# Kernel tuning notes

Hardware: AMD Instinct MI355X
Metric: run time of the kernel (lower is better)

Reference implementation:

```python
import jax, jax.numpy as jnp
import numpy as np
from jax import lax

B, T, D = 4, 2048, 2048
H, K, V = 16, 128, 128
CONV_K = 4
EPS_G = 1e-6
LN_EPS = 1e-5


def _dconv_causal(x, w, b):
    # x: (B,T,C); w: (C,1,Kk) depthwise. torch pads both sides Kk-1 then slices [:T],
    # which equals a causal left-pad of Kk-1.
    y = lax.conv_general_dilated(
        jnp.transpose(x, (0, 2, 1)), w, (1,),
        [(w.shape[-1] - 1, 0)],
        dimension_numbers=('NCH', 'OIH', 'NCH'),
        feature_group_count=w.shape[0])
    return jnp.transpose(y + b[None, :, None], (0, 2, 1))


def _kda_scan(q, k, v, g, beta, scale):
    # q,k: (B,H,T,K); v: (B,H,T,V); g: (B,H,T,K) log-decay (channel-wise); beta: (B,H,T)
    # Gated delta rule: S_t = Diag(exp(g_t)) S_{t-1} + beta_t k_t (v_t - k_t^T Diag(exp(g_t)) S_{t-1})
    S0 = jnp.zeros(q.shape[:2] + (q.shape[-1], v.shape[-1]), q.dtype)

    def step(S, inp):
        qt, kt, vt, gt, bt = inp
        S = S * jnp.exp(gt)[..., :, None]                     # per-key-channel decay
        err = vt - jnp.einsum('bhk,bhkv->bhv', kt, S)         # delta correction
        S = S + bt[..., None, None] * kt[..., None] * err[..., None, :]
        o = scale * jnp.einsum('bhk,bhkv->bhv', qt, S)
        return S, o

    xs = tuple(jnp.moveaxis(t_, 2, 0) for t_ in (q, k, v, g)) + (jnp.moveaxis(beta, 2, 0),)
    _, o = lax.scan(step, S0, xs)
    return jnp.moveaxis(o, 0, 2)                              # (B,H,T,V)


def setup_inputs() -> dict:
    key = jax.random.key(0)
    ks = jax.random.split(key, 16)
    s = 0.02
    return {
        'x':   jax.random.normal(ks[0], (B, T, D), jnp.float32),
        'Wq':  jax.random.normal(ks[1], (H * K, D), jnp.float32) * s,
        'Wk':  jax.random.normal(ks[2], (H * K, D), jnp.float32) * s,
        'Wv':  jax.random.normal(ks[3], (H * V, D), jnp.float32) * s,
        'Wa':  jax.random.normal(ks[4], (H * V, D), jnp.float32) * s,
        'ba':  jax.random.normal(ks[5], (H * V,), jnp.float32) * s,
        'Wb':  jax.random.normal(ks[6], (H, D), jnp.float32) * s,
        'bb':  jax.random.normal(ks[7], (H,), jnp.float32) * s,
        'Wg':  jax.random.normal(ks[8], (H * V, D), jnp.float32) * s,
        'Wo':  jax.random.normal(ks[9], (D, H * V), jnp.float32) * s,
        'cqw': jax.random.normal(ks[10], (H * K, 1, CONV_K), jnp.float32) * 0.2,
        'cqb': jnp.zeros((H * K,), jnp.float32),
        'ckw': jax.random.normal(ks[11], (H * K, 1, CONV_K), jnp.float32) * 0.2,
        'ckb': jnp.zeros((H * K,), jnp.float32),
        'cvw': jax.random.normal(ks[12], (H * V, 1, CONV_K), jnp.float32) * 0.2,
        'cvb': jnp.zeros((H * V,), jnp.float32),
        'ln_w': jnp.ones((V,), jnp.float32),
        'ln_b': jnp.zeros((V,), jnp.float32),
    }


def reference(x, Wq, Wk, Wv, Wa, ba, Wb, bb, Wg, Wo,
              cqw, cqb, ckw, ckb, cvw, cvb, ln_w, ln_b):
    b, t, _ = x.shape
    scale = K ** -0.5
    q = jax.nn.silu(_dconv_causal(x @ Wq.T, cqw, cqb))
    k = jax.nn.silu(_dconv_causal(x @ Wk.T, ckw, ckb))
    v = jax.nn.silu(_dconv_causal(x @ Wv.T, cvw, cvb))
    q = q.reshape(b, t, H, K).transpose(0, 2, 1, 3)           # (B,H,T,K)
    k = k.reshape(b, t, H, K).transpose(0, 2, 1, 3)
    v = v.reshape(b, t, H, V).transpose(0, 2, 1, 3)
    a = jax.nn.sigmoid(x @ Wa.T + ba).reshape(b, t, H, V).transpose(0, 2, 1, 3)
    g = jnp.log(jnp.maximum(a, EPS_G))                        # log-space channel gate
    beta = jax.nn.sigmoid(x @ Wb.T + bb).transpose(0, 2, 1)   # (B,H,T)
    o = _kda_scan(q, k, v, g, beta, scale).transpose(0, 2, 1, 3)  # (B,T,H,V)
    mu = o.mean(-1, keepdims=True)
    var = ((o - mu) ** 2).mean(-1, keepdims=True)
    o = (o - mu) * lax.rsqrt(var + LN_EPS) * ln_w + ln_b      # per-head LayerNorm
    gate = jax.nn.sigmoid(x @ Wg.T).reshape(b, t, H, V)
    return ((o * gate).reshape(b, t, H * V)) @ Wo.T
```

## Files before the change

kernel.cpp:

```cpp
#include <hip/hip_runtime.h>
#include <cstdint>
#include <cstddef>

#define B_ 4
#define T_ 2048
#define D_ 2048
#define H_ 16

typedef __bf16 bf16x8 __attribute__((ext_vector_type(8)));
typedef float  f32x4  __attribute__((ext_vector_type(4)));
typedef unsigned short u16;
typedef u16 u16x8 __attribute__((ext_vector_type(8)));

__device__ __forceinline__ u16 f2bf(float f) {
    union { float f; unsigned u; } v; v.f = f;
    unsigned r = v.u + 0x7FFFu + ((v.u >> 16) & 1u);
    return (u16)(r >> 16);
}
__device__ __forceinline__ float bf2f(u16 h) {
    union { unsigned u; float f; } v; v.u = ((unsigned)h) << 16;
    return v.f;
}
__device__ __forceinline__ float sigmoidf_(float x) {
    return 1.f / (1.f + __expf(-x));
}
__device__ __forceinline__ void async_load16(const void* g, void* l) {
    __builtin_amdgcn_global_load_lds(
        (const __attribute__((address_space(1))) void*)g,
        (__attribute__((address_space(3))) void*)l,
        16, 0, 0);
}

__device__ __forceinline__ float row_allreduce16(float x) {
    int v;
    v = __builtin_amdgcn_update_dpp(0, __builtin_bit_cast(int, x), 0xB1, 0xF, 0xF, true);
    x += __builtin_bit_cast(float, v);
    v = __builtin_amdgcn_update_dpp(0, __builtin_bit_cast(int, x), 0x4E, 0xF, 0xF, true);
    x += __builtin_bit_cast(float, v);
    v = __builtin_amdgcn_update_dpp(0, __builtin_bit_cast(int, x), 0x140, 0xF, 0xF, true);
    x += __builtin_bit_cast(float, v);
    v = __builtin_amdgcn_update_dpp(0, __builtin_bit_cast(int, x), 0x141, 0xF, 0xF, true);
    x += __builtin_bit_cast(float, v);
    return x;
}

__global__ void cvt_bf16_k(const float* __restrict__ s, u16* __restrict__ d, int n) {
    int i = blockIdx.x * 256 + threadIdx.x;
    if (i * 4 < n) {
        float4 v = *(const float4*)(s + (size_t)i * 4);
        ushort4 o = {f2bf(v.x), f2bf(v.y), f2bf(v.z), f2bf(v.w)};
        *(ushort4*)(d + (size_t)i * 4) = o;
    }
}

__global__ void pad_wb_k(const float* __restrict__ Wb, u16* __restrict__ d) {
    int i = blockIdx.x * 256 + threadIdx.x;
    d[i] = (i < 32768) ? f2bf(Wb[i]) : (u16)0;
}

__device__ __forceinline__ void store_c(float* p, float v) { *p = v; }
__device__ __forceinline__ void store_c(u16* p, float v) { *p = f2bf(v); }

template <typename OutT, int PERM>
__global__ __launch_bounds__(256) void gemm_bt(const u16* __restrict__ A,
                                               const u16* __restrict__ Bm,
                                               OutT* __restrict__ C, int K, int ldc) {
    __shared__ __align__(16) u16 smA[128 * 64];
    __shared__ __align__(16) u16 smB[128 * 64];
    const int tid  = threadIdx.x;
    const int lane = tid & 63;
    const int w    = tid >> 6;
    const int wm   = (w >> 1) * 64;
    const int wn   = (w & 1) * 64;
    const int bm   = blockIdx.x, bn = blockIdx.y;

    f32x4 acc[4][4];
#pragma unroll
    for (int i = 0; i < 4; ++i)
#pragma unroll
        for (int j = 0; j < 4; ++j) acc[i][j] = (f32x4){0.f, 0.f, 0.f, 0.f};

    const int rr = tid >> 3;
    const int cc = (tid & 7) * 8;
    const u16* Ag = A + (size_t)(bm * 128) * K;
    const u16* Bg = Bm + (size_t)(bn * 128) * K;

    for (int k0 = 0; k0 < K; k0 += 64) {
#pragma unroll
        for (int it = 0; it < 4; ++it) {
            async_load16(Ag + (size_t)(it * 32 + rr) * K + (k0 + cc), &smA[(it * 256 + tid) * 8]);
            async_load16(Bg + (size_t)(it * 32 + rr) * K + (k0 + cc), &smB[(it * 256 + tid) * 8]);
        }
        __syncthreads();
#pragma unroll
        for (int kk = 0; kk < 64; kk += 32) {
            bf16x8 af[4], bfr[4];
            const int qoff = kk + ((lane >> 4) * 8);
#pragma unroll
            for (int mi = 0; mi < 4; ++mi)
                af[mi] = *(const bf16x8*)&smA[(wm + mi * 16 + (lane & 15)) * 64 + qoff];
#pragma unroll
            for (int ni = 0; ni < 4; ++ni)
                bfr[ni] = *(const bf16x8*)&smB[(wn + ni * 16 + (lane & 15)) * 64 + qoff];
#pragma unroll
            for (int mi = 0; mi < 4; ++mi)
#pragma unroll
                for (int ni = 0; ni < 4; ++ni)
                    acc[mi][ni] = __builtin_amdgcn_mfma_f32_16x16x32_bf16(af[mi], bfr[ni], acc[mi][ni], 0, 0, 0);
        }
        __syncthreads();
    }

#pragma unroll
    for (int mi = 0; mi < 4; ++mi) {
        const int row0 = bm * 128 + wm + mi * 16 + ((lane >> 4) * 4);
#pragma unroll
        for (int ni = 0; ni < 4; ++ni) {
            int colg = bn * 128 + wn + ni * 16 + (lane & 15);
            if (PERM) colg = (colg & ~127) | (((colg & 15) << 3) | ((colg >> 4) & 7));
#pragma unroll
            for (int rg = 0; rg < 4; ++rg)
                store_c(&C[(size_t)(row0 + rg) * ldc + colg], acc[mi][ni][rg]);
        }
    }
}

template <int TRANSPOSE>
__global__ void conv_silu_k(const u16* __restrict__ pre,
                            const float* __restrict__ w, const float* __restrict__ bias,
                            u16* __restrict__ outp) {
    int idx = blockIdx.x * 256 + threadIdx.x;
    int c = idx & 2047;
    int t = (idx >> 11) & (T_ - 1);
    int b = idx >> 22;
    const u16* base = pre + (size_t)(b * T_ + t) * 2048 + c;
    float acc = bias[c];
#pragma unroll
    for (int j = 0; j < 4; ++j) {
        int tt = t - 3 + j;
        if (tt >= 0) {
            float xv = bf2f(base[(ptrdiff_t)(j - 3) * 2048]);
            acc = fmaf(xv, w[c * 4 + j], acc);
        }
    }
    float y = acc * sigmoidf_(acc);
    int h = c >> 7, cl = c & 127;
    int p = TRANSPOSE ? ((cl & 15) * 8 + (cl >> 4)) : cl;
    outp[((size_t)(b * H_ + h) * T_ + t) * 128 + p] = f2bf(y);
}

#define TB2 16
__global__ __launch_bounds__(512, 2) void kda_scan_k(const u16* __restrict__ qg,
                                                     const u16* __restrict__ kg,
                                                     const u16* __restrict__ vg,
                                                     const u16* __restrict__ ag,
                                                     const u16* __restrict__ bpg,
                                                     const float* __restrict__ bav,
                                                     const float* __restrict__ bbv,
                                                     u16* __restrict__ og) {
    const int blk = blockIdx.x;
    const int xcd = blk & 7;
    const int ci  = (blk >> 3) & 7;
    const int vch = blk >> 6;
    const int bh  = xcd * 8 + ci;
    const int tid = threadIdx.x;
    const int lane = tid & 63;
    const int w    = tid >> 6;
    const int colIdx = w * 4 + (lane >> 4);
    const int sl     = lane & 15;
    const int b = bh >> 4, h = bh & 15;

    __shared__ __align__(16) u16   sq[2][TB2][128];
    __shared__ __align__(16) u16   sk[2][TB2][128];
    __shared__ __align__(16) float sdA[2][TB2][64];
    __shared__ __align__(16) float sdB[2][TB2][64];
    __shared__ float sv[2][TB2][32];
    __shared__ float sb_[2][TB2];

    const u16* qb  = qg + (size_t)bh * T_ * 128;
    const u16* kb  = kg + (size_t)bh * T_ * 128;
    const u16* vst = vg + (size_t)bh * T_ * 128 + vch * 32 + (tid & 31);
    const u16* ab  = ag + (size_t)b * T_ * 2048 + h * 128;
    const u16* bpb = bpg + (size_t)b * T_ * 128 + h;
    u16* op = og + (size_t)b * T_ * 2048 + h * 128 + vch * 32 + colIdx;

    const int ur = tid >> 5;
    const int c4 = (tid & 31) * 4;
    const int chb = c4 >> 3;
    const int jb  = c4 & 7;
    const float rba0 = bav[h * 128 + (jb + 0) * 16 + chb];
    const float rba1 = bav[h * 128 + (jb + 1) * 16 + chb];
    const float rba2 = bav[h * 128 + (jb + 2) * 16 + chb];
    const float rba3 = bav[h * 128 + (jb + 3) * 16 + chb];
    const float bbh = bbv[h];
    float* dst_d = (c4 & 4) ? &sdB[0][0][0] : &sdA[0][0][0];
    const int doff = ur * 64 + chb * 4;
    const int dstride = TB2 * 64;

    float S[8];
#pragma unroll
    for (int j = 0; j < 8; ++j) S[j] = 0.f;

    ushort4 rq = *(const ushort4*)(qb + (size_t)ur * 128 + c4);
    ushort4 rk = *(const ushort4*)(kb + (size_t)ur * 128 + c4);
    ushort4 ra = *(const ushort4*)(ab + (size_t)ur * 2048 + c4);
    u16 rv = vst[(size_t)ur * 128];
    float rbet = (tid < TB2) ? bf2f(bpb[(size_t)tid * 128]) : 0.f;

    const float scale = 0.08838834764831845f;
    const int NM = T_ / TB2;
    for (int m = 0; m < NM; ++m) {
        const int pb = m & 1;
        float4 fd = {fmaxf(sigmoidf_(bf2f(ra.x) + rba0), 1e-6f),
                     fmaxf(sigmoidf_(bf2f(ra.y) + rba1), 1e-6f),
                     fmaxf(sigmoidf_(bf2f(ra.z) + rba2), 1e-6f),
                     fmaxf(sigmoidf_(bf2f(ra.w) + rba3), 1e-6f)};
        *(ushort4*)&sq[pb][ur][c4] = rq;
        *(ushort4*)&sk[pb][ur][c4] = rk;
        *(float4*)(dst_d + pb * dstride + doff) = fd;
        sv[pb][ur][tid & 31] = bf2f(rv);
        if (tid < TB2) sb_[pb][tid] = sigmoidf_(rbet + bbh);
        __syncthreads();
        if (m + 1 < NM) {
            size_t t0n = (size_t)(m + 1) * TB2;
            rq = *(const ushort4*)(qb + (t0n + ur) * 128 + c4);
            rk = *(const ushort4*)(kb + (t0n + ur) * 128 + c4);
            ra = *(const ushort4*)(ab + (t0n + ur) * 2048 + c4);
            rv = vst[(t0n + ur) * 128];
            if (tid < TB2) rbet = bf2f(bpb[(t0n + tid) * 128]);
        }
        u16x8  q8c = *(const u16x8*)&sq[pb][0][sl * 8];
        u16x8  k8c = *(const u16x8*)&sk[pb][0][sl * 8];
        float4 dAc = *(const float4*)&sdA[pb][0][sl * 4];
        float4 dBc = *(const float4*)&sdB[pb][0][sl * 4];
        float  fvc = sv[pb][0][colIdx];
        float  sbc = sb_[pb][0];
#pragma unroll
        for (int u = 0; u < TB2; ++u) {
            u16x8 q8n, k8n; float4 dAn, dBn; float fvn = 0.f, sbn = 0.f;
            if (u + 1 < TB2) {
                q8n = *(const u16x8*)&sq[pb][u + 1][sl * 8];
                k8n = *(const u16x8*)&sk[pb][u + 1][sl * 8];
                dAn = *(const float4*)&sdA[pb][u + 1][sl * 4];
                dBn = *(const float4*)&sdB[pb][u + 1][sl * 4];
                fvn = sv[pb][u + 1][colIdx];
                sbn = sb_[pb][u + 1];
            }
            float qf[8], kf[8], dv[8];
#pragma unroll
            for (int j = 0; j < 8; ++j) { kf[j] = bf2f(k8c[j]); qf[j] = bf2f(q8c[j]); }
            dv[0] = dAc.x; dv[1] = dAc.y; dv[2] = dAc.z; dv[3] = dAc.w;
            dv[4] = dBc.x; dv[5] = dBc.y; dv[6] = dBc.z; dv[7] = dBc.w;
            float e0 = 0.f, e1 = 0.f;
#pragma unroll
            for (int j = 0; j < 8; j += 2) {
                S[j]     *= dv[j];     e0 = fmaf(kf[j],     S[j],     e0);
                S[j + 1] *= dv[j + 1]; e1 = fmaf(kf[j + 1], S[j + 1], e1);
            }
            float errp = row_allreduce16(e0 + e1);
            float uu = sbc * (fvc - errp);
            float o0 = 0.f, o1 = 0.f;
#pragma unroll
            for (int j = 0; j < 8; j += 2) {
                S[j]     = fmaf(kf[j],     uu, S[j]);     o0 = fmaf(qf[j],     S[j],     o0);
                S[j + 1] = fmaf(kf[j + 1], uu, S[j + 1]); o1 = fmaf(qf[j + 1], S[j + 1], o1);
            }
            float outv = row_allreduce16(o0 + o1);
            if (sl == 0)
                op[(size_t)(m * TB2 + u) * 2048] = f2bf(scale * outv);
            if (u + 1 < TB2) {
                q8c = q8n; k8c = k8n; dAc = dAn; dBc = dBn; fvc = fvn; sbc = sbn;
            }
        }
        __syncthreads();
    }
}

__global__ __launch_bounds__(256) void ln_gate_k(const u16* __restrict__ o,
                                                 const u16* __restrict__ gpre,
                                                 const float* __restrict__ lnw,
                                                 const float* __restrict__ lnb,
                                                 u16* __restrict__ act) {
    int inst = blockIdx.x * 4 + (threadIdx.x >> 6);
    int lane = threadIdx.x & 63;
    int bt = inst >> 4, h = inst & 15;
    const u16* opr = o + (size_t)bt * 2048 + h * 128;
    ushort2 xr = *(const ushort2*)(opr + lane * 2);
    float x0 = bf2f(xr.x), x1 = bf2f(xr.y);
    float s  = x0 + x1;
    float ss = x0 * x0 + x1 * x1;
#pragma unroll
    for (int msk = 1; msk < 64; msk <<= 1) {
        s  += __shfl_xor(s, msk);
        ss += __shfl_xor(ss, msk);
    }
    float mu   = s * (1.f / 128.f);
    float var  = ss * (1.f / 128.f) - mu * mu;
    float rstd = rsqrtf(var + 1e-5f);
    const u16* gp = gpre + (size_t)bt * 2048 + h * 128 + lane * 2;
    u16* ap = act + (size_t)bt * 2048 + h * 128 + lane * 2;
#pragma unroll
    for (int e = 0; e < 2; ++e) {
        int v = lane * 2 + e;
        float xx = (e == 0) ? x0 : x1;
        float y = (xx - mu) * rstd * lnw[v] + lnb[v];
        float gate = sigmoidf_(bf2f(gp[e]));
        ap[e] = f2bf(y * gate);
    }
}

extern "C" void kernel_launch(void* const* d_in, const int* in_sizes, int n_in,
                              void* d_out, int out_size, void* d_ws, size_t ws_size,
                              hipStream_t stream) {
    (void)in_sizes; (void)n_in; (void)out_size; (void)ws_size;
    const float* x   = (const float*)d_in[0];
    const float* Wq  = (const float*)d_in[1];
    const float* Wk  = (const float*)d_in[2];
    const float* Wv  = (const float*)d_in[3];
    const float* Wa  = (const float*)d_in[4];
    const float* ba  = (const float*)d_in[5];
    const float* Wb  = (const float*)d_in[6];
    const float* bbv = (const float*)d_in[7];
    const float* Wg  = (const float*)d_in[8];
    const float* Wo  = (const float*)d_in[9];
    const float* cqw = (const float*)d_in[10];
    const float* cqb = (const float*)d_in[11];
    const float* ckw = (const float*)d_in[12];
    const float* ckb = (const float*)d_in[13];
    const float* cvw = (const float*)d_in[14];
    const float* cvb = (const float*)d_in[15];
    const float* lnw = (const float*)d_in[16];
    const float* lnb = (const float*)d_in[17];
    float* out = (float*)d_out;

    char* p = (char*)d_ws;
    size_t off = 0;
    auto take = [&](size_t bytes) -> char* {
        char* r = p + off;
        off += (bytes + 255) & ~(size_t)255;
        return r;
    };
    u16* Wslot = (u16*)take((size_t)4194304 * 2);
    u16* qpre  = (u16*)take((size_t)16777216 * 2);
    u16* kpre  = (u16*)take((size_t)16777216 * 2);
    u16* vpre  = (u16*)take((size_t)16777216 * 2);
    u16* apre  = (u16*)take((size_t)16777216 * 2);
    u16* bpre  = (u16*)take((size_t)1048576 * 2);

    u16* xb  = (u16*)d_out;
    u16* qsc = (u16*)d_out + 16777216;
    u16* ksc  = qpre;
    u16* vsc  = kpre;
    u16* ob   = vpre;
    u16* gpre = qpre;
    u16* act  = kpre;

    cvt_bf16_k<<<16384, 256, 0, stream>>>(x, xb, 16777216);

    cvt_bf16_k<<<4096, 256, 0, stream>>>(Wq, Wslot, 4194304);
    gemm_bt<u16, 0><<<dim3(64, 16), 256, 0, stream>>>(xb, Wslot, qpre, 2048, 2048);
    cvt_bf16_k<<<4096, 256, 0, stream>>>(Wk, Wslot, 4194304);
    gemm_bt<u16, 0><<<dim3(64, 16), 256, 0, stream>>>(xb, Wslot, kpre, 2048, 2048);
    cvt_bf16_k<<<4096, 256, 0, stream>>>(Wv, Wslot, 4194304);
    gemm_bt<u16, 0><<<dim3(64, 16), 256, 0, stream>>>(xb, Wslot, vpre, 2048, 2048);
    cvt_bf16_k<<<4096, 256, 0, stream>>>(Wa, Wslot, 4194304);
    gemm_bt<u16, 1><<<dim3(64, 16), 256, 0, stream>>>(xb, Wslot, apre, 2048, 2048);
    pad_wb_k<<<1024, 256, 0, stream>>>(Wb, Wslot);
    gemm_bt<u16, 0><<<dim3(64, 1), 256, 0, stream>>>(xb, Wslot, bpre, 2048, 128);

    conv_silu_k<1><<<65536, 256, 0, stream>>>(qpre, cqw, cqb, qsc);
    conv_silu_k<1><<<65536, 256, 0, stream>>>(kpre, ckw, ckb, ksc);
    conv_silu_k<0><<<65536, 256, 0, stream>>>(vpre, cvw, cvb, vsc);

    kda_scan_k<<<256, 512, 0, stream>>>(qsc, ksc, vsc, apre, bpre, ba, bbv, ob);

    cvt_bf16_k<<<4096, 256, 0, stream>>>(Wg, Wslot, 4194304);
    gemm_bt<u16, 0><<<dim3(64, 16), 256, 0, stream>>>(xb, Wslot, gpre, 2048, 2048);

    ln_gate_k<<<32768, 256, 0, stream>>>(ob, gpre, lnw, lnb, act);

    cvt_bf16_k<<<4096, 256, 0, stream>>>(Wo, Wslot, 4194304);
    gemm_bt<float, 0><<<dim3(64, 16), 256, 0, stream>>>(act, Wslot, out, 2048, 2048);
}
```

Before: 1.661 ms.

## Give each scan thread two value columns and halve the block size

```diff
diff --git a/kernel.cpp b/kernel.cpp
--- a/kernel.cpp
+++ b/kernel.cpp
@@ -150,7 +150,7 @@
 }
 
 #define TB2 16
-__global__ __launch_bounds__(512, 2) void kda_scan_k(const u16* __restrict__ qg,
+__global__ __launch_bounds__(256, 1) void kda_scan_k(const u16* __restrict__ qg,
                                                      const u16* __restrict__ kg,
                                                      const u16* __restrict__ vg,
                                                      const u16* __restrict__ ag,
@@ -166,8 +166,9 @@
     const int tid = threadIdx.x;
     const int lane = tid & 63;
     const int w    = tid >> 6;
-    const int colIdx = w * 4 + (lane >> 4);
-    const int sl     = lane & 15;
+    const int cs   = lane >> 4;
+    const int c0   = w * 4 + cs;
+    const int sl   = lane & 15;
     const int b = bh >> 4, h = bh & 15;
 
     __shared__ __align__(16) u16   sq[2][TB2][128];
@@ -179,10 +180,9 @@
 
     const u16* qb  = qg + (size_t)bh * T_ * 128;
     const u16* kb  = kg + (size_t)bh * T_ * 128;
-    const u16* vst = vg + (size_t)bh * T_ * 128 + vch * 32 + (tid & 31);
     const u16* ab  = ag + (size_t)b * T_ * 2048 + h * 128;
     const u16* bpb = bpg + (size_t)b * T_ * 128 + h;
-    u16* op = og + (size_t)b * T_ * 2048 + h * 128 + vch * 32 + colIdx;
+    u16* op = og + (size_t)b * T_ * 2048 + h * 128 + vch * 32 + c0;
 
     const int ur = tid >> 5;
     const int c4 = (tid & 31) * 4;
@@ -196,80 +196,111 @@
     float* dst_d = (c4 & 4) ? &sdB[0][0][0] : &sdA[0][0][0];
     const int doff = ur * 64 + chb * 4;
     const int dstride = TB2 * 64;
-
-    float S[8];
-#pragma unroll
-    for (int j = 0; j < 8; ++j) S[j] = 0.f;
-
-    ushort4 rq = *(const ushort4*)(qb + (size_t)ur * 128 + c4);
-    ushort4 rk = *(const ushort4*)(kb + (size_t)ur * 128 + c4);
-    ushort4 ra = *(const ushort4*)(ab + (size_t)ur * 2048 + c4);
-    u16 rv = vst[(size_t)ur * 128];
+    const int vr = tid >> 4;
+    const int vc = tid & 15;
+    const u16* vst = vg + (size_t)bh * T_ * 128 + vch * 32 + vc;
+
+    float S0[8], S1[8];
+#pragma unroll
+    for (int j = 0; j < 8; ++j) { S0[j] = 0.f; S1[j] = 0.f; }
+
+    ushort4 rq0 = *(const ushort4*)(qb + (size_t)ur * 128 + c4);
+    ushort4 rq1 = *(const ushort4*)(qb + (size_t)(ur + 8) * 128 + c4);
+    ushort4 rk0 = *(const ushort4*)(kb + (size_t)ur * 128 + c4);
+    ushort4 rk1 = *(const ushort4*)(kb + (size_t)(ur + 8) * 128 + c4);
+    ushort4 ra0 = *(const ushort4*)(ab + (size_t)ur * 2048 + c4);
+    ushort4 ra1 = *(const ushort4*)(ab + (size_t)(ur + 8) * 2048 + c4);
+    u16 rv0 = vst[(size_t)vr * 128];
+    u16 rv1 = vst[(size_t)vr * 128 + 16];
     float rbet = (tid < TB2) ? bf2f(bpb[(size_t)tid * 128]) : 0.f;
 
     const float scale = 0.08838834764831845f;
     const int NM = T_ / TB2;
     for (int m = 0; m < NM; ++m) {
         const int pb = m & 1;
-        float4 fd = {fmaxf(sigmoidf_(bf2f(ra.x) + rba0), 1e-6f),
-                     fmaxf(sigmoidf_(bf2f(ra.y) + rba1), 1e-6f),
-                     fmaxf(sigmoidf_(bf2f(ra.z) + rba2), 1e-6f),
-                     fmaxf(sigmoidf_(bf2f(ra.w) + rba3), 1e-6f)};
-        *(ushort4*)&sq[pb][ur][c4] = rq;
-        *(ushort4*)&sk[pb][ur][c4] = rk;
-        *(float4*)(dst_d + pb * dstride + doff) = fd;
-        sv[pb][ur][tid & 31] = bf2f(rv);
+        float4 fd0 = {fmaxf(sigmoidf_(bf2f(ra0.x) + rba0), 1e-6f),
+                      fmaxf(sigmoidf_(bf2f(ra0.y) + rba1), 1e-6f),
+                      fmaxf(sigmoidf_(bf2f(ra0.z) + rba2), 1e-6f),
+                      fmaxf(sigmoidf_(bf2f(ra0.w) + rba3), 1e-6f)};
+        float4 fd1 = {fmaxf(sigmoidf_(bf2f(ra1.x) + rba0), 1e-6f),
+                      fmaxf(sigmoidf_(bf2f(ra1.y) + rba1), 1e-6f),
+                      fmaxf(sigmoidf_(bf2f(ra1.z) + rba2), 1e-6f),
+                      fmaxf(sigmoidf_(bf2f(ra1.w) + rba3), 1e-6f)};
+        *(ushort4*)&sq[pb][ur][c4]     = rq0;
+        *(ushort4*)&sq[pb][ur + 8][c4] = rq1;
+        *(ushort4*)&sk[pb][ur][c4]     = rk0;
+        *(ushort4*)&sk[pb][ur + 8][c4] = rk1;
+        *(float4*)(dst_d + pb * dstride + doff)       = fd0;
+        *(float4*)(dst_d + pb * dstride + doff + 512) = fd1;
+        sv[pb][vr][vc]      = bf2f(rv0);
+        sv[pb][vr][vc + 16] = bf2f(rv1);
         if (tid < TB2) sb_[pb][tid] = sigmoidf_(rbet + bbh);
         __syncthreads();
         if (m + 1 < NM) {
             size_t t0n = (size_t)(m + 1) * TB2;
-            rq = *(const ushort4*)(qb + (t0n + ur) * 128 + c4);
-            rk = *(const ushort4*)(kb + (t0n + ur) * 128 + c4);
-            ra = *(const ushort4*)(ab + (t0n + ur) * 2048 + c4);
-            rv = vst[(t0n + ur) * 128];
+            rq0 = *(const ushort4*)(qb + (t0n + ur) * 128 + c4);
+            rq1 = *(const ushort4*)(qb + (t0n + ur + 8) * 128 + c4);
+            rk0 = *(const ushort4*)(kb + (t0n + ur) * 128 + c4);
+            rk1 = *(const ushort4*)(kb + (t0n + ur + 8) * 128 + c4);
+            ra0 = *(const ushort4*)(ab + (t0n + ur) * 2048 + c4);
+            ra1 = *(const ushort4*)(ab + (t0n + ur + 8) * 2048 + c4);
+            rv0 = vst[(t0n + vr) * 128];
+            rv1 = vst[(t0n + vr) * 128 + 16];
             if (tid < TB2) rbet = bf2f(bpb[(t0n + tid) * 128]);
         }
         u16x8  q8c = *(const u16x8*)&sq[pb][0][sl * 8];
         u16x8  k8c = *(const u16x8*)&sk[pb][0][sl * 8];
         float4 dAc = *(const float4*)&sdA[pb][0][sl * 4];
         float4 dBc = *(const float4*)&sdB[pb][0][sl * 4];
-        float  fvc = sv[pb][0][colIdx];
-        float  sbc = sb_[pb][0];
+        float  fv0c = sv[pb][0][c0];
+        float  fv1c = sv[pb][0][c0 + 16];
+        float  sbc  = sb_[pb][0];
 #pragma unroll
         for (int u = 0; u < TB2; ++u) {
-            u16x8 q8n, k8n; float4 dAn, dBn; float fvn = 0.f, sbn = 0.f;
+            u16x8 q8n, k8n; float4 dAn, dBn; float fv0n = 0.f, fv1n = 0.f, sbn = 0.f;
             if (u + 1 < TB2) {
                 q8n = *(const u16x8*)&sq[pb][u + 1][sl * 8];
                 k8n = *(const u16x8*)&sk[pb][u + 1][sl * 8];
                 dAn = *(const float4*)&sdA[pb][u + 1][sl * 4];
                 dBn = *(const float4*)&sdB[pb][u + 1][sl * 4];
-                fvn = sv[pb][u + 1][colIdx];
-                sbn = sb_[pb][u + 1];
+                fv0n = sv[pb][u + 1][c0];
+                fv1n = sv[pb][u + 1][c0 + 16];
+                sbn  = sb_[pb][u + 1];
             }
             float qf[8], kf[8], dv[8];
 #pragma unroll
             for (int j = 0; j < 8; ++j) { kf[j] = bf2f(k8c[j]); qf[j] = bf2f(q8c[j]); }
             dv[0] = dAc.x; dv[1] = dAc.y; dv[2] = dAc.z; dv[3] = dAc.w;
             dv[4] = dBc.x; dv[5] = dBc.y; dv[6] = dBc.z; dv[7] = dBc.w;
-            float e0 = 0.f, e1 = 0.f;
+            float e00 = 0.f, e01 = 0.f, e10 = 0.f, e11 = 0.f;
 #pragma unroll
             for (int j = 0; j < 8; j += 2) {
-                S[j]     *= dv[j];     e0 = fmaf(kf[j],     S[j],     e0);
-                S[j + 1] *= dv[j + 1]; e1 = fmaf(kf[j + 1], S[j + 1], e1);
+                S0[j]     *= dv[j];     e00 = fmaf(kf[j],     S0[j],     e00);
+                S1[j]     *= dv[j];     e10 = fmaf(kf[j],     S1[j],     e10);
+                S0[j + 1] *= dv[j + 1]; e01 = fmaf(kf[j + 1], S0[j + 1], e01);
+                S1[j + 1] *= dv[j + 1]; e11 = fmaf(kf[j + 1], S1[j + 1], e11);
             }
-            float errp = row_allreduce16(e0 + e1);
-            float uu = sbc * (fvc - errp);
-            float o0 = 0.f, o1 = 0.f;
+            float errp0 = row_allreduce16(e00 + e01);
+            float errp1 = row_allreduce16(e10 + e11);
+            float uu0 = sbc * (fv0c - errp0);
+            float uu1 = sbc * (fv1c - errp1);
+            float o00 = 0.f, o01 = 0.f, o10 = 0.f, o11 = 0.f;
 #pragma unroll
             for (int j = 0; j < 8; j += 2) {
-                S[j]     = fmaf(kf[j],     uu, S[j]);     o0 = fmaf(qf[j],     S[j],     o0);
-                S[j + 1] = fmaf(kf[j + 1], uu, S[j + 1]); o1 = fmaf(qf[j + 1], S[j + 1], o1);
+                S0[j]     = fmaf(kf[j],     uu0, S0[j]);     o00 = fmaf(qf[j],     S0[j],     o00);
+                S1[j]     = fmaf(kf[j],     uu1, S1[j]);     o10 = fmaf(qf[j],     S1[j],     o10);
+                S0[j + 1] = fmaf(kf[j + 1], uu0, S0[j + 1]); o01 = fmaf(qf[j + 1], S0[j + 1], o01);
+                S1[j + 1] = fmaf(kf[j + 1], uu1, S1[j + 1]); o11 = fmaf(qf[j + 1], S1[j + 1], o11);
             }
-            float outv = row_allreduce16(o0 + o1);
-            if (sl == 0)
-                op[(size_t)(m * TB2 + u) * 2048] = f2bf(scale * outv);
+            float outv0 = row_allreduce16(o00 + o01);
+            float outv1 = row_allreduce16(o10 + o11);
+            if (sl == 0) {
+                op[(size_t)(m * TB2 + u) * 2048]      = f2bf(scale * outv0);
+                op[(size_t)(m * TB2 + u) * 2048 + 16] = f2bf(scale * outv1);
+            }
             if (u + 1 < TB2) {
-                q8c = q8n; k8c = k8n; dAc = dAn; dBc = dBn; fvc = fvn; sbc = sbn;
+                q8c = q8n; k8c = k8n; dAc = dAn; dBc = dBn;
+                fv0c = fv0n; fv1c = fv1n; sbc = sbn;
             }
         }
         __syncthreads();
@@ -372,7 +403,7 @@
     conv_silu_k<1><<<65536, 256, 0, stream>>>(kpre, ckw, ckb, ksc);
     conv_silu_k<0><<<65536, 256, 0, stream>>>(vpre, cvw, cvb, vsc);
 
-    kda_scan_k<<<256, 512, 0, stream>>>(qsc, ksc, vsc, apre, bpre, ba, bbv, ob);
+    kda_scan_k<<<256, 256, 0, stream>>>(qsc, ksc, vsc, apre, bpre, ba, bbv, ob);
 
     cvt_bf16_k<<<4096, 256, 0, stream>>>(Wg, Wslot, 4194304);
     gemm_bt<u16, 0><<<dim3(64, 16), 256, 0, stream>>>(xb, Wslot, gpre, 2048, 2048);
```

Measured after the change: 1.702 ms. 2.5% more time.
